# Optimization experiments

Measured on AMD Instinct MI355X. Metric: run time of the kernel, lower is better.

The kernel has to match this reference:

```python
import jax, jax.numpy as jnp
import numpy as np

B, T, D, K = 64, 1024, 256, 1024
DECAY = 0.99      # ema_decay
BETA = 0.25       # commitment_cost
EPS = 1e-5


def setup_inputs() -> dict:
    key = jax.random.key(0)
    k1, k2 = jax.random.split(key, 2)
    z = jax.random.normal(k1, (B, T, D), dtype=jnp.float32)
    # nn.init.uniform_(embedding.weight, -1/K, 1/K)
    embed = jax.random.uniform(k2, (K, D), dtype=jnp.float32,
                               minval=-1.0 / K, maxval=1.0 / K)
    ema_count = jnp.zeros((K,), dtype=jnp.float32)
    ema_weight = embed  # buffer initialized as a clone of the weight
    return {"z": z, "embed": embed, "ema_count": ema_count, "ema_weight": ema_weight}


def reference(z, embed, ema_count, ema_weight):
    Bq, Tq, Dq = z.shape
    zf = z.reshape(-1, Dq)  # [N, D], N = B*T
    # squared euclidean distances: [N, K]
    dist = (zf * zf).sum(axis=1, keepdims=True) \
        - 2.0 * (zf @ embed.T) \
        + (embed * embed).sum(axis=1)
    idx = jnp.argmin(dist, axis=1)                      # [N]
    q = embed[idx].reshape(Bq, Tq, Dq)                  # nearest codebook vectors

    commit = jnp.mean((z - jax.lax.stop_gradient(q)) ** 2)
    codebook = jnp.mean((q - jax.lax.stop_gradient(z)) ** 2)
    vq_loss = codebook + BETA * commit

    # straight-through estimator
    q_st = z + jax.lax.stop_gradient(q - z)

    # EMA codebook update (training-mode, no_grad in torch)
    counts = jax.ops.segment_sum(jnp.ones((zf.shape[0],), zf.dtype), idx, num_segments=K)
    dw = jax.ops.segment_sum(zf, idx, num_segments=K)   # one_hot.T @ z_flat, [K, D]
    new_count = DECAY * ema_count + (1.0 - DECAY) * counts
    new_ema_w = DECAY * ema_weight + (1.0 - DECAY) * dw
    n = new_count.sum()
    cs = (new_count + EPS) / (n + K * EPS) * n          # laplace-smoothed counts
    new_embed = new_ema_w / cs[:, None]

    return (q_st, vq_loss, idx.reshape(Bq, Tq), new_embed, new_count, new_ema_w)
```

## Files before the change

### kernel.cpp

```cpp
#include <hip/hip_runtime.h>
#include <cfloat>

#define N_Q     65536
#define D_DIM   256
#define K_CODES 1024
#define DELTA   0.004f
#define MARGIN  0.001f
#define SW_CAP  1536
#define SPILL_CAP 65536

#define OUT_QST   0
#define OUT_LOSS  16777216
#define OUT_IDX   16777217
#define OUT_EMBED 16842753
#define OUT_COUNT 17104897
#define OUT_EMAW  17105921

#define WS_IDX    0u
#define WS_ZZ     262144u
#define WS_PERM   524288u
#define WS_PACK   786432u
#define WS_EN     1310720u
#define WS_ICNT   1314816u
#define WS_OFFS   1318912u
#define WS_OFFW   1323008u
#define WS_CNTF   1327104u
#define WS_CS     1331200u
#define WS_ET     1335296u
#define WS_LOSSB  1859584u
#define WS_SPCNT  1867776u

typedef short          bf16x8 __attribute__((ext_vector_type(8)));
typedef unsigned short u16x8  __attribute__((ext_vector_type(8)));
typedef float          f32x4  __attribute__((ext_vector_type(4)));

__device__ inline unsigned short f2bf(float x) {
    unsigned u = __float_as_uint(x);
    u += 0x7FFFu + ((u >> 16) & 1u);
    return (unsigned short)(u >> 16);
}
__device__ inline float bf2f(unsigned short h) {
    return __uint_as_float((unsigned)h << 16);
}
__device__ inline u16x8 pack8(float4 a, float4 b) {
    u16x8 p;
    p[0]=f2bf(a.x); p[1]=f2bf(a.y); p[2]=f2bf(a.z); p[3]=f2bf(a.w);
    p[4]=f2bf(b.x); p[5]=f2bf(b.y); p[6]=f2bf(b.z); p[7]=f2bf(b.w);
    return p;
}
__device__ inline void gll16(const void* g, void* l) {
    __builtin_amdgcn_global_load_lds(
        (const __attribute__((address_space(1))) unsigned int*)g,
        (__attribute__((address_space(3))) unsigned int*)l, 16, 0, 0);
}
#define SWZMIN(x, PAT) fminf((x), __int_as_float( \
    __builtin_amdgcn_ds_swizzle(__float_as_int(x), (PAT))))

__global__ void prep_kernel(const float* __restrict__ embed,
                            unsigned short* __restrict__ et,
                            unsigned long long* __restrict__ pack,
                            float* __restrict__ enorm,
                            int* __restrict__ icnt,
                            double* __restrict__ lossb,
                            int* __restrict__ spc)
{
    int b = blockIdx.x, t = threadIdx.x;
    if (b < 128) {
        int tid = b * 256 + t;
        int k16 = tid >> 9, d8 = (tid >> 4) & 31, col = tid & 15;
        const float* src = &embed[(size_t)(k16 * 16 + col) * D_DIM + d8 * 8];
        float4 a = *(const float4*)&src[0];
        float4 c = *(const float4*)&src[4];
        *(u16x8*)&et[(size_t)tid * 8] = pack8(a, c);
        unsigned long long* p = pack + (size_t)tid * 2;
        p[0] = ~0ull; p[1] = ~0ull;
    } else {
        int b2 = b - 128;
        int wave = t >> 6, lane = t & 63;
        int rbase = (b2 * 4 + wave) * 8;
        for (int i = 0; i < 8; ++i) {
            int r = rbase + i;
            const float4 v = *(const float4*)&embed[(size_t)r * D_DIM + lane * 4];
            float s = v.x * v.x + v.y * v.y + v.z * v.z + v.w * v.w;
            #pragma unroll
            for (int m = 32; m >= 1; m >>= 1) s += __shfl_down(s, m, 64);
            if (lane == 0) enorm[r] = s;
        }
        if (b2 == 0) {
            #pragma unroll
            for (int i = 0; i < 4; ++i) {
                icnt[t * 4 + i] = 0;
                lossb[t * 4 + i] = 0.0;
            }
            if (t == 0) *spc = 0;
        }
    }
}

__launch_bounds__(256, 2)
__global__ void sweep_kernel(const float* __restrict__ z,
                             const float* __restrict__ embed,
                             const unsigned short* __restrict__ et,
                             const float* __restrict__ enorm,
                             float* __restrict__ zzg,
                             unsigned long long* __restrict__ pack,
                             unsigned* __restrict__ spill,
                             int* __restrict__ spc)
{
    __shared__ unsigned short Eb[2][16384];
    __shared__ unsigned list[SW_CAP];
    __shared__ unsigned short s1h[SW_CAP];
    __shared__ float Ens[K_CODES];
    __shared__ float rminS[128];
    __shared__ float zzS[128];
    __shared__ int lcnt;

    const int t = threadIdx.x;
    const int w = t >> 6, lane = t & 63;
    const int col = lane & 15, quad = lane >> 4;
    const int qbase = blockIdx.x * 128;

    if (t == 0) lcnt = 0;
    for (int i = t; i < K_CODES; i += 256) Ens[i] = enorm[i];

    {
        const unsigned short* src = et + w * 4096 + lane * 8;
        unsigned short* dst = &Eb[0][w * 4096];
        #pragma unroll
        for (int i = 0; i < 8; ++i) gll16(src + i * 512, dst + i * 512);
    }

    bf16x8 A[2][8];
    #pragma unroll
    for (int rt = 0; rt < 2; ++rt) {
        float s = 0.f;
        #pragma unroll
        for (int ds = 0; ds < 8; ++ds) {
            const float* zp = &z[(size_t)(qbase + w*32 + rt*16 + col) * D_DIM
                                 + ds*32 + quad*8];
            float4 a = *(const float4*)zp;
            float4 b = *(const float4*)(zp + 4);
            s += a.x*a.x + a.y*a.y + a.z*a.z + a.w*a.w
               + b.x*b.x + b.y*b.y + b.z*b.z + b.w*b.w;
            u16x8 p = pack8(a, b);
            A[rt][ds] = *(bf16x8*)&p;
        }
        s += __shfl_xor(s, 16, 64);
        s += __shfl_xor(s, 32, 64);
        if (quad == 0) {
            zzg[qbase + w*32 + rt*16 + col] = s;
            zzS[w*32 + rt*16 + col] = s;
        }
    }

    float rmin[8];
    #pragma unroll
    for (int i = 0; i < 8; ++i) rmin[i] = FLT_MAX;

    __syncthreads();

    #pragma unroll 1
    for (int kc = 0; kc < 16; ++kc) {
        if (kc < 15) {
            const unsigned short* src = et + (kc + 1) * 16384 + w * 4096 + lane * 8;
            unsigned short* dst = &Eb[(kc + 1) & 1][w * 4096];
            #pragma unroll
            for (int i = 0; i < 8; ++i) gll16(src + i * 512, dst + i * 512);
        }

        const unsigned short* buf = Eb[kc & 1];
        f32x4 acc[2][4];
        #pragma unroll
        for (int rt = 0; rt < 2; ++rt)
            #pragma unroll
            for (int ct = 0; ct < 4; ++ct)
                acc[rt][ct] = (f32x4){0.f, 0.f, 0.f, 0.f};

        #pragma unroll
        for (int ds = 0; ds < 8; ++ds) {
            bf16x8 B[4];
            #pragma unroll
            for (int ct = 0; ct < 4; ++ct)
                B[ct] = *(const bf16x8*)&buf[((ct*32 + ds*4 + quad)*16 + col)*8];
            #pragma unroll
            for (int ct = 0; ct < 4; ++ct) {
                acc[0][ct] = __builtin_amdgcn_mfma_f32_16x16x32_bf16(A[0][ds], B[ct], acc[0][ct], 0, 0, 0);
                acc[1][ct] = __builtin_amdgcn_mfma_f32_16x16x32_bf16(A[1][ds], B[ct], acc[1][ct], 0, 0, 0);
            }
        }

        float en4[4];
        #pragma unroll
        for (int ct = 0; ct < 4; ++ct) en4[ct] = Ens[kc*64 + ct*16 + col];

        float s1v[2][4][4];
        #pragma unroll
        for (int rt = 0; rt < 2; ++rt)
            #pragma unroll
            for (int ct = 0; ct < 4; ++ct)
                #pragma unroll
                for (int rg = 0; rg < 4; ++rg)
                    s1v[rt][ct][rg] = fmaf(-2.0f, acc[rt][ct][rg], en4[ct]);

        float m8[8];
        #pragma unroll
        for (int rt = 0; rt < 2; ++rt)
            #pragma unroll
            for (int rg = 0; rg < 4; ++rg)
                m8[rt*4+rg] = fminf(fminf(s1v[rt][0][rg], s1v[rt][1][rg]),
                                    fminf(s1v[rt][2][rg], s1v[rt][3][rg]));

        #pragma unroll
        for (int i = 0; i < 8; ++i) m8[i] = SWZMIN(m8[i], 0x041F);
        #pragma unroll
        for (int i = 0; i < 8; ++i) m8[i] = SWZMIN(m8[i], 0x081F);
        #pragma unroll
        for (int i = 0; i < 8; ++i) m8[i] = SWZMIN(m8[i], 0x101F);
        #pragma unroll
        for (int i = 0; i < 8; ++i) m8[i] = SWZMIN(m8[i], 0x201F);

        float thrv[8];
        #pragma unroll
        for (int i = 0; i < 8; ++i) {
            rmin[i] = fminf(rmin[i], m8[i]);
            thrv[i] = rmin[i] + DELTA;
        }

        #pragma unroll
        for (int rt = 0; rt < 2; ++rt)
            #pragma unroll
            for (int rg = 0; rg < 4; ++rg) {
                float th = thrv[rt*4+rg];
                #pragma unroll
                for (int ct = 0; ct < 4; ++ct) {
                    if (s1v[rt][ct][rg] <= th) {
                        int k    = kc*64 + ct*16 + col;
                        int qloc = w*32 + rt*16 + quad*4 + rg;
                        int pos  = atomicAdd(&lcnt, 1);
                        if (pos < SW_CAP) {
                            list[pos] = ((unsigned)qloc << 10) | (unsigned)k;
                            s1h[pos]  = f2bf(s1v[rt][ct][rg]);
                        } else {
                            int sp = atomicAdd(spc, 1);
                            if (sp < SPILL_CAP)
                                spill[sp] = ((unsigned)(qbase + qloc) << 10)
                                          | (unsigned)k;
                        }
                    }
                }
            }

        __syncthreads();
    }

    if (col == 0) {
        #pragma unroll
        for (int rt = 0; rt < 2; ++rt)
            #pragma unroll
            for (int rg = 0; rg < 4; ++rg)
                rminS[w*32 + rt*16 + quad*4 + rg] = rmin[rt*4+rg];
    }
    __syncthreads();

    int cnt = min(lcnt, SW_CAP);
    int gid = t >> 3, gl = t & 7;
    for (int e = gid; e < cnt; e += 32) {
        unsigned ent = list[e];
        int qloc = (int)(ent >> 10), k = (int)(ent & 1023u);
        if (bf2f(s1h[e]) > rminS[qloc] + (DELTA + MARGIN)) continue;
        int qg = qbase + qloc;
        const float* zp  = &z[(size_t)qg * D_DIM + gl * 32];
        const float* epf = &embed[(size_t)k * D_DIM + gl * 32];
        double d0 = 0.0, d1 = 0.0;
        #pragma unroll
        for (int i = 0; i < 4; ++i) {
            float4 a  = *(const float4*)&zp[i*8];
            float4 b  = *(const float4*)&epf[i*8];
            float4 c  = *(const float4*)&zp[i*8 + 4];
            float4 dv = *(const float4*)&epf[i*8 + 4];
            d0 += (double)a.x*b.x + (double)a.y*b.y + (double)a.z*b.z + (double)a.w*b.w;
            d1 += (double)c.x*dv.x + (double)c.y*dv.y + (double)c.z*dv.z + (double)c.w*dv.w;
        }
        double dd = d0 + d1;
        #pragma unroll
        for (int m = 1; m < 8; m <<= 1) dd += __shfl_xor(dd, m, 64);
        if (gl == 0) {
            float s = (zzS[qloc] - 2.0f*(float)dd) + Ens[k];
            unsigned long long pk =
                ((unsigned long long)__float_as_uint(s) << 32) | (unsigned)k;
            atomicMin(&pack[qg], pk);
        }
    }
}

__global__ void spill_kernel(const float* __restrict__ z,
                             const float* __restrict__ embed,
                             const float* __restrict__ enorm,
                             const float* __restrict__ zz,
                             const unsigned* __restrict__ spill,
                             const int* __restrict__ spc,
                             unsigned long long* __restrict__ pack)
{
    int cnt = *spc; if (cnt > SPILL_CAP) cnt = SPILL_CAP;
    int gid = (blockIdx.x * 256 + threadIdx.x) >> 3, gl = threadIdx.x & 7;
    int stride = (gridDim.x * 256) >> 3;
    for (int e = gid; e < cnt; e += stride) {
        unsigned ent = spill[e];
        int qg = (int)(ent >> 10), k = (int)(ent & 1023u);
        const float* zp  = &z[(size_t)qg * D_DIM + gl * 32];
        const float* epf = &embed[(size_t)k * D_DIM + gl * 32];
        double dd = 0.0;
        #pragma unroll
        for (int i = 0; i < 8; ++i) {
            float4 a = *(const float4*)&zp[i*4];
            float4 b = *(const float4*)&epf[i*4];
            dd += (double)a.x*b.x + (double)a.y*b.y
                + (double)a.z*b.z + (double)a.w*b.w;
        }
        #pragma unroll
        for (int m = 1; m < 8; m <<= 1) dd += __shfl_xor(dd, m, 64);
        if (gl == 0) {
            float s = (zz[qg] - 2.0f*(float)dd) + enorm[k];
            unsigned long long pk =
                ((unsigned long long)__float_as_uint(s) << 32) | (unsigned)k;
            atomicMin(&pack[qg], pk);
        }
    }
}

__global__ void unpack_kernel(const unsigned long long* __restrict__ pack,
                              int* __restrict__ idx_i,
                              float* __restrict__ idx_f,
                              int* __restrict__ icnt)
{
    int n = blockIdx.x * 256 + threadIdx.x;
    int k = (int)(pack[n] & 0xffffffffull);
    idx_i[n] = k;
    idx_f[n] = (float)k;
    atomicAdd(&icnt[k], 1);
}

__global__ void scan_kernel(const int* __restrict__ icnt,
                            int* __restrict__ offs,
                            int* __restrict__ offw,
                            float* __restrict__ cntf)
{
    __shared__ int s[1024];
    int t = threadIdx.x;
    int v0 = icnt[t];
    s[t] = v0;
    __syncthreads();
    for (int d = 1; d < 1024; d <<= 1) {
        int v = (t >= d) ? s[t - d] : 0;
        __syncthreads();
        s[t] += v;
        __syncthreads();
    }
    int excl = s[t] - v0;
    offs[t] = excl;
    offw[t] = excl;
    cntf[t] = (float)v0;
}

__global__ void fill_kernel(const int* __restrict__ idx,
                            int* __restrict__ offw,
                            int* __restrict__ perm)
{
    int n = blockIdx.x * 256 + threadIdx.x;
    int k = idx[n];
    int pos = atomicAdd(&offw[k], 1);
    perm[pos] = n;
}

__global__ void qst_loss_kernel(const float* __restrict__ z,
                                const float* __restrict__ embed,
                                const int* __restrict__ idx,
                                float* __restrict__ qst,
                                double* __restrict__ lossb)
{
    int tid = blockIdx.x * blockDim.x + threadIdx.x;
    int e0  = tid * 4;
    int n   = e0 >> 8, d = e0 & 255;
    int k   = idx[n];
    const float4 q4 = *(const float4*)&embed[(size_t)k * D_DIM + d];
    const float4 z4 = *(const float4*)&z[e0];
    float4 o;
    o.x = z4.x + (q4.x - z4.x);
    o.y = z4.y + (q4.y - z4.y);
    o.z = z4.z + (q4.z - z4.z);
    o.w = z4.w + (q4.w - z4.w);
    *(float4*)&qst[e0] = o;
    float dx = z4.x - q4.x, dy = z4.y - q4.y, dz = z4.z - q4.z, dw = z4.w - q4.w;
    float s = dx * dx + dy * dy + dz * dz + dw * dw;
    #pragma unroll
    for (int m = 32; m >= 1; m >>= 1) s += __shfl_down(s, m, 64);
    __shared__ float ps[4];
    int wave = threadIdx.x >> 6, lane = threadIdx.x & 63;
    if (lane == 0) ps[wave] = s;
    __syncthreads();
    if (threadIdx.x == 0)
        atomicAdd(&lossb[blockIdx.x & 1023],
                  (double)((ps[0] + ps[1]) + (ps[2] + ps[3])));
}

__global__ void fin_counts_kernel(const float* __restrict__ ema_count,
                                  const float* __restrict__ cntf,
                                  const double* __restrict__ lossb,
                                  float* __restrict__ out_count,
                                  float* __restrict__ out_loss,
                                  float* __restrict__ cs)
{
    __shared__ float  red[1024];
    __shared__ double dred[1024];
    int t = threadIdx.x;
    float c = 0.99f * ema_count[t] + 0.01f * cntf[t];
    out_count[t] = c;
    red[t]  = c;
    dred[t] = lossb[t];
    __syncthreads();
    for (int s = 512; s >= 1; s >>= 1) {
        if (t < s) { red[t] += red[t + s]; dred[t] += dred[t + s]; }
        __syncthreads();
    }
    float n = red[0];
    cs[t] = (c + 1e-5f) / (n + 1024.0f * 1e-5f) * n;
    if (t == 0) {
        float m = (float)(dred[0] / (double)((size_t)N_Q * D_DIM));
        out_loss[0] = m + 0.25f * m;
    }
}

__global__ void accum_embed_kernel(const float* __restrict__ z,
                                   const int* __restrict__ perm,
                                   const int* __restrict__ icnt,
                                   const int* __restrict__ offs,
                                   const float* __restrict__ cs,
                                   const float* __restrict__ ema_w,
                                   float* __restrict__ out_embed,
                                   float* __restrict__ out_emaw)
{
    __shared__ int rows[256];
    int k = blockIdx.x, t = threadIdx.x;
    int cnt = icnt[k], off = offs[k];
    double a0 = 0.0, a1 = 0.0, a2 = 0.0, a3 = 0.0;
    for (int base = 0; base < cnt; base += 256) {
        int m = min(256, cnt - base);
        __syncthreads();
        if (t < m) rows[t] = perm[off + base + t];
        __syncthreads();
        int r = 0;
        for (; r + 4 <= m; r += 4) {
            a0 += (double)z[(size_t)rows[r+0] * D_DIM + t];
            a1 += (double)z[(size_t)rows[r+1] * D_DIM + t];
            a2 += (double)z[(size_t)rows[r+2] * D_DIM + t];
            a3 += (double)z[(size_t)rows[r+3] * D_DIM + t];
        }
        for (; r < m; ++r) a0 += (double)z[(size_t)rows[r] * D_DIM + t];
    }
    double acc = (a0 + a1) + (a2 + a3);
    float w = 0.99f * ema_w[(size_t)k * D_DIM + t] + 0.01f * (float)acc;
    out_emaw[(size_t)k * D_DIM + t]  = w;
    out_embed[(size_t)k * D_DIM + t] = w / cs[k];
}

extern "C" void kernel_launch(void* const* d_in, const int* in_sizes, int n_in,
                              void* d_out, int out_size, void* d_ws, size_t ws_size,
                              hipStream_t stream)
{
    const float* z          = (const float*)d_in[0];
    const float* embed      = (const float*)d_in[1];
    const float* ema_count  = (const float*)d_in[2];
    const float* ema_weight = (const float*)d_in[3];
    float* out = (float*)d_out;
    char*  ws  = (char*)d_ws;

    int*      ws_idx  = (int*)(ws + WS_IDX);
    unsigned* ws_spill= (unsigned*)(ws + WS_IDX);
    float*    ws_zz   = (float*)(ws + WS_ZZ);
    int*      ws_perm = (int*)(ws + WS_PERM);
    unsigned long long* ws_pack = (unsigned long long*)(ws + WS_PACK);
    float*    ws_en   = (float*)(ws + WS_EN);
    int*      ws_icnt = (int*)(ws + WS_ICNT);
    int*      ws_offs = (int*)(ws + WS_OFFS);
    int*      ws_offw = (int*)(ws + WS_OFFW);
    float*    ws_cntf = (float*)(ws + WS_CNTF);
    float*    ws_cs   = (float*)(ws + WS_CS);
    unsigned short* ws_et = (unsigned short*)(ws + WS_ET);
    double*   ws_lb   = (double*)(ws + WS_LOSSB);
    int*      ws_spc  = (int*)(ws + WS_SPCNT);

    prep_kernel<<<160, 256, 0, stream>>>(embed, ws_et, ws_pack, ws_en,
                                         ws_icnt, ws_lb, ws_spc);

    sweep_kernel<<<N_Q / 128, 256, 0, stream>>>(z, embed, ws_et, ws_en, ws_zz,
                                                ws_pack, ws_spill, ws_spc);

    spill_kernel<<<32, 256, 0, stream>>>(z, embed, ws_en, ws_zz,
                                         ws_spill, ws_spc, ws_pack);

    unpack_kernel<<<N_Q / 256, 256, 0, stream>>>(ws_pack, ws_idx,
                                                 out + OUT_IDX, ws_icnt);
    scan_kernel<<<1, 1024, 0, stream>>>(ws_icnt, ws_offs, ws_offw, ws_cntf);
    fill_kernel<<<N_Q / 256, 256, 0, stream>>>(ws_idx, ws_offw, ws_perm);
    qst_loss_kernel<<<(N_Q * (D_DIM / 4)) / 256, 256, 0, stream>>>(
        z, embed, ws_idx, out + OUT_QST, ws_lb);
    fin_counts_kernel<<<1, 1024, 0, stream>>>(ema_count, ws_cntf, ws_lb,
                                              out + OUT_COUNT, out + OUT_LOSS, ws_cs);
    accum_embed_kernel<<<K_CODES, 256, 0, stream>>>(z, ws_perm, ws_icnt, ws_offs,
                                                    ws_cs, ema_weight,
                                                    out + OUT_EMBED, out + OUT_EMAW);
}
```

Before: 298.4 us.

## Run sweep kernel with 512 threads, one 16-row tile per wave, explicit barriers

The sweep kernel now launches 512 threads per block, so each of 8 waves handles 16 query rows instead of 32. This halves per-thread accumulators and registers and doubles the waves available to hide latency. __syncthreads is replaced by manual s_waitcnt vmcnt(4) plus s_barrier, so the prefetch of the next codebook chunk can stay in flight across the barrier. The risks are more LDS B-fragment reads per MFMA, since each B load now feeds one MFMA instead of two, and fragile manual waitcnt correctness.

```diff
diff --git a/kernel.cpp b/kernel.cpp
--- a/kernel.cpp
+++ b/kernel.cpp
@@ -97,7 +97,7 @@
     }
 }
 
-__launch_bounds__(256, 2)
+__launch_bounds__(512, 4)
 __global__ void sweep_kernel(const float* __restrict__ z,
                              const float* __restrict__ embed,
                              const unsigned short* __restrict__ et,
@@ -121,60 +121,59 @@
     const int qbase = blockIdx.x * 128;
 
     if (t == 0) lcnt = 0;
-    for (int i = t; i < K_CODES; i += 256) Ens[i] = enorm[i];
+    for (int i = t; i < K_CODES; i += 512) Ens[i] = enorm[i];
 
     {
-        const unsigned short* src = et + w * 4096 + lane * 8;
-        unsigned short* dst = &Eb[0][w * 4096];
-        #pragma unroll
-        for (int i = 0; i < 8; ++i) gll16(src + i * 512, dst + i * 512);
-    }
-
-    bf16x8 A[2][8];
-    #pragma unroll
-    for (int rt = 0; rt < 2; ++rt) {
+        const unsigned short* src = et + w * 2048 + lane * 8;
+        unsigned short* dst = &Eb[0][w * 2048];
+        #pragma unroll
+        for (int i = 0; i < 4; ++i) gll16(src + i * 512, dst + i * 512);
+    }
+
+    bf16x8 A[8];
+    {
         float s = 0.f;
         #pragma unroll
         for (int ds = 0; ds < 8; ++ds) {
-            const float* zp = &z[(size_t)(qbase + w*32 + rt*16 + col) * D_DIM
+            const float* zp = &z[(size_t)(qbase + w*16 + col) * D_DIM
                                  + ds*32 + quad*8];
             float4 a = *(const float4*)zp;
             float4 b = *(const float4*)(zp + 4);
             s += a.x*a.x + a.y*a.y + a.z*a.z + a.w*a.w
                + b.x*b.x + b.y*b.y + b.z*b.z + b.w*b.w;
             u16x8 p = pack8(a, b);
-            A[rt][ds] = *(bf16x8*)&p;
+            A[ds] = *(bf16x8*)&p;
         }
         s += __shfl_xor(s, 16, 64);
         s += __shfl_xor(s, 32, 64);
         if (quad == 0) {
-            zzg[qbase + w*32 + rt*16 + col] = s;
-            zzS[w*32 + rt*16 + col] = s;
-        }
-    }
-
-    float rmin[8];
+            zzg[qbase + w*16 + col] = s;
+            zzS[w*16 + col] = s;
+        }
+    }
+
+    float rmin[4];
     #pragma unroll
-    for (int i = 0; i < 8; ++i) rmin[i] = FLT_MAX;
-
-    __syncthreads();
+    for (int i = 0; i < 4; ++i) rmin[i] = FLT_MAX;
+
+    asm volatile("s_waitcnt vmcnt(0) lgkmcnt(0)" ::: "memory");
+    __builtin_amdgcn_s_barrier();
+    __builtin_amdgcn_sched_barrier(0);
 
     #pragma unroll 1
     for (int kc = 0; kc < 16; ++kc) {
         if (kc < 15) {
-            const unsigned short* src = et + (kc + 1) * 16384 + w * 4096 + lane * 8;
-            unsigned short* dst = &Eb[(kc + 1) & 1][w * 4096];
-            #pragma unroll
-            for (int i = 0; i < 8; ++i) gll16(src + i * 512, dst + i * 512);
+            const unsigned short* src = et + (kc + 1) * 16384 + w * 2048 + lane * 8;
+            unsigned short* dst = &Eb[(kc + 1) & 1][w * 2048];
+            #pragma unroll
+            for (int i = 0; i < 4; ++i) gll16(src + i * 512, dst + i * 512);
         }
 
         const unsigned short* buf = Eb[kc & 1];
-        f32x4 acc[2][4];
-        #pragma unroll
-        for (int rt = 0; rt < 2; ++rt)
-            #pragma unroll
-            for (int ct = 0; ct < 4; ++ct)
-                acc[rt][ct] = (f32x4){0.f, 0.f, 0.f, 0.f};
+        f32x4 acc[4];
+        #pragma unroll
+        for (int ct = 0; ct < 4; ++ct)
+            acc[ct] = (f32x4){0.f, 0.f, 0.f, 0.f};
 
         #pragma unroll
         for (int ds = 0; ds < 8; ++ds) {
@@ -183,88 +182,85 @@
             for (int ct = 0; ct < 4; ++ct)
                 B[ct] = *(const bf16x8*)&buf[((ct*32 + ds*4 + quad)*16 + col)*8];
             #pragma unroll
+            for (int ct = 0; ct < 4; ++ct)
+                acc[ct] = __builtin_amdgcn_mfma_f32_16x16x32_bf16(A[ds], B[ct], acc[ct], 0, 0, 0);
+        }
+
+        float en4[4];
+        #pragma unroll
+        for (int ct = 0; ct < 4; ++ct) en4[ct] = Ens[kc*64 + ct*16 + col];
+
+        float s1v[4][4];
+        #pragma unroll
+        for (int ct = 0; ct < 4; ++ct)
+            #pragma unroll
+            for (int rg = 0; rg < 4; ++rg)
+                s1v[ct][rg] = fmaf(-2.0f, acc[ct][rg], en4[ct]);
+
+        float m4[4];
+        #pragma unroll
+        for (int rg = 0; rg < 4; ++rg)
+            m4[rg] = fminf(fminf(s1v[0][rg], s1v[1][rg]),
+                           fminf(s1v[2][rg], s1v[3][rg]));
+
+        #pragma unroll
+        for (int i = 0; i < 4; ++i) m4[i] = SWZMIN(m4[i], 0x041F);
+        #pragma unroll
+        for (int i = 0; i < 4; ++i) m4[i] = SWZMIN(m4[i], 0x081F);
+        #pragma unroll
+        for (int i = 0; i < 4; ++i) m4[i] = SWZMIN(m4[i], 0x101F);
+        #pragma unroll
+        for (int i = 0; i < 4; ++i) m4[i] = SWZMIN(m4[i], 0x201F);
+
+        float thrv[4];
+        #pragma unroll
+        for (int i = 0; i < 4; ++i) {
+            rmin[i] = fminf(rmin[i], m4[i]);
+            thrv[i] = rmin[i] + DELTA;
+        }
+
+        #pragma unroll
+        for (int rg = 0; rg < 4; ++rg) {
+            float th = thrv[rg];
+            #pragma unroll
             for (int ct = 0; ct < 4; ++ct) {
-                acc[0][ct] = __builtin_amdgcn_mfma_f32_16x16x32_bf16(A[0][ds], B[ct], acc[0][ct], 0, 0, 0);
-                acc[1][ct] = __builtin_amdgcn_mfma_f32_16x16x32_bf16(A[1][ds], B[ct], acc[1][ct], 0, 0, 0);
-            }
-        }
-
-        float en4[4];
-        #pragma unroll
-        for (int ct = 0; ct < 4; ++ct) en4[ct] = Ens[kc*64 + ct*16 + col];
-
-        float s1v[2][4][4];
-        #pragma unroll
-        for (int rt = 0; rt < 2; ++rt)
-            #pragma unroll
-            for (int ct = 0; ct < 4; ++ct)
-                #pragma unroll
-                for (int rg = 0; rg < 4; ++rg)
-                    s1v[rt][ct][rg] = fmaf(-2.0f, acc[rt][ct][rg], en4[ct]);
-
-        float m8[8];
-        #pragma unroll
-        for (int rt = 0; rt < 2; ++rt)
-            #pragma unroll
-            for (int rg = 0; rg < 4; ++rg)
-                m8[rt*4+rg] = fminf(fminf(s1v[rt][0][rg], s1v[rt][1][rg]),
-                                    fminf(s1v[rt][2][rg], s1v[rt][3][rg]));
-
-        #pragma unroll
-        for (int i = 0; i < 8; ++i) m8[i] = SWZMIN(m8[i], 0x041F);
-        #pragma unroll
-        for (int i = 0; i < 8; ++i) m8[i] = SWZMIN(m8[i], 0x081F);
-        #pragma unroll
-        for (int i = 0; i < 8; ++i) m8[i] = SWZMIN(m8[i], 0x101F);
-        #pragma unroll
-        for (int i = 0; i < 8; ++i) m8[i] = SWZMIN(m8[i], 0x201F);
-
-        float thrv[8];
-        #pragma unroll
-        for (int i = 0; i < 8; ++i) {
-            rmin[i] = fminf(rmin[i], m8[i]);
-            thrv[i] = rmin[i] + DELTA;
-        }
-
-        #pragma unroll
-        for (int rt = 0; rt < 2; ++rt)
-            #pragma unroll
-            for (int rg = 0; rg < 4; ++rg) {
-                float th = thrv[rt*4+rg];
-                #pragma unroll
-                for (int ct = 0; ct < 4; ++ct) {
-                    if (s1v[rt][ct][rg] <= th) {
-                        int k    = kc*64 + ct*16 + col;
-                        int qloc = w*32 + rt*16 + quad*4 + rg;
-                        int pos  = atomicAdd(&lcnt, 1);
-                        if (pos < SW_CAP) {
-                            list[pos] = ((unsigned)qloc << 10) | (unsigned)k;
-                            s1h[pos]  = f2bf(s1v[rt][ct][rg]);
-                        } else {
-                            int sp = atomicAdd(spc, 1);
-                            if (sp < SPILL_CAP)
-                                spill[sp] = ((unsigned)(qbase + qloc) << 10)
-                                          | (unsigned)k;
+                if (s1v[ct][rg] <= th) {
+                    int k    = kc*64 + ct*16 + col;
+                    int qloc = w*16 + quad*4 + rg;
+                    int pos  = atomicAdd(&lcnt, 1);
+                    if (pos < SW_CAP) {
+                        list[pos] = ((unsigned)qloc << 10) | (unsigned)k;
+                        s1h[pos]  = f2bf(s1v[ct][rg]);
+                    } else {
+                        int sp = atomicAdd(spc, 1);
+                        if (sp < SPILL_CAP) {
+                            spill[sp] = ((unsigned)(qbase + qloc) << 10)
+                                      | (unsigned)k;
+                            asm volatile("s_waitcnt vmcnt(0)" ::: "memory");
                         }
                     }
                 }
             }
-
-        __syncthreads();
+        }
+
+        asm volatile("s_waitcnt vmcnt(4)" ::: "memory");
+        __builtin_amdgcn_s_barrier();
+        __builtin_amdgcn_sched_barrier(0);
     }
 
     if (col == 0) {
         #pragma unroll
-        for (int rt = 0; rt < 2; ++rt)
-            #pragma unroll
-            for (int rg = 0; rg < 4; ++rg)
-                rminS[w*32 + rt*16 + quad*4 + rg] = rmin[rt*4+rg];
-    }
-    __syncthreads();
-
-    int cnt = min(lcnt, SW_CAP);
+        for (int rg = 0; rg < 4; ++rg)
+            rminS[w*16 + quad*4 + rg] = rmin[rg];
+    }
+    asm volatile("s_waitcnt lgkmcnt(0)" ::: "memory");
+    __builtin_amdgcn_s_barrier();
+    __builtin_amdgcn_sched_barrier(0);
+    asm volatile("" ::: "memory");
+
+    int cnt = lcnt; if (cnt > SW_CAP) cnt = SW_CAP;
     int gid = t >> 3, gl = t & 7;
-    for (int e = gid; e < cnt; e += 32) {
+    for (int e = gid; e < cnt; e += 64) {
         unsigned ent = list[e];
         int qloc = (int)(ent >> 10), k = (int)(ent & 1023u);
         if (bf2f(s1h[e]) > rminS[qloc] + (DELTA + MARGIN)) continue;
@@ -492,7 +488,7 @@
     prep_kernel<<<160, 256, 0, stream>>>(embed, ws_et, ws_pack, ws_en,
                                          ws_icnt, ws_lb, ws_spc);
 
-    sweep_kernel<<<N_Q / 128, 256, 0, stream>>>(z, embed, ws_et, ws_en, ws_zz,
+    sweep_kernel<<<N_Q / 128, 512, 0, stream>>>(z, embed, ws_et, ws_en, ws_zz,
                                                 ws_pack, ws_spill, ws_spc);
 
     spill_kernel<<<32, 256, 0, stream>>>(z, embed, ws_en, ws_zz,
```

New measurement: 284.7 us. -4.6%, faster.
